# Performance work log

Hardware: AMD Instinct MI355X
Metric: run time of the kernel (lower is better)

## Reference

```python
import jax, jax.numpy as jnp
import numpy as np

N = 4096
HIDDEN = 256
NUM_HEADS = 8
HEAD_DIM = HIDDEN // NUM_HEADS
LN_EPS = 1e-3


def setup_inputs() -> dict:
    key = jax.random.key(0)
    ks = jax.random.split(key, 8)
    s = 1.0 / np.sqrt(HIDDEN)
    feat = jax.random.normal(ks[0], (N, HIDDEN), dtype=jnp.float32)
    Wq = jax.random.normal(ks[1], (HIDDEN, HIDDEN), dtype=jnp.float32) * s
    bq = jnp.zeros((HIDDEN,), dtype=jnp.float32)
    Wkv = jax.random.normal(ks[2], (HIDDEN, 2 * HIDDEN), dtype=jnp.float32) * s
    bkv = jnp.zeros((2 * HIDDEN,), dtype=jnp.float32)
    Weg = jax.random.normal(ks[3], (HIDDEN, 2 * NUM_HEADS), dtype=jnp.float32) * s
    beg = jnp.zeros((2 * NUM_HEADS,), dtype=jnp.float32)
    ln_g = jnp.ones((HIDDEN,), dtype=jnp.float32)
    ln_b = jnp.zeros((HIDDEN,), dtype=jnp.float32)
    return {"feat": feat, "Wq": Wq, "bq": bq, "Wkv": Wkv, "bkv": bkv,
            "Weg": Weg, "beg": beg, "ln_g": ln_g, "ln_b": ln_b}


def reference(feat, Wq, bq, Wkv, bkv, Weg, beg, ln_g, ln_b):
    n = feat.shape[0]
    # projections
    Q = feat @ Wq + bq                                  # [N, hidden]
    KV = feat @ Wkv + bkv                               # [N, 2*hidden]
    K, V = jnp.split(KV, 2, axis=-1)
    EG = feat @ Weg + beg                               # [N, 2*heads]
    E, G = jnp.split(EG, 2, axis=-1)                    # each [N, heads]
    # reshape to [N, head_dim, heads] (heads is the FAST axis, as in torch .view)
    Q = Q.reshape(n, HEAD_DIM, NUM_HEADS) * (HEAD_DIM ** -0.5)
    K = K.reshape(n, HEAD_DIM, NUM_HEADS)
    V = V.reshape(n, HEAD_DIM, NUM_HEADS)
    # all-pairs scores with per-j edge bias: [N, N, heads]
    H = jnp.einsum('idh,jdh->ijh', Q, K) + E[None, :, :]
    # softmax over i (axis 0), post-softmax sigmoid gate (per j, h)
    A = jax.nn.softmax(H, axis=0) * jax.nn.sigmoid(G)[None, :, :]
    Va = jnp.einsum('ijh,jdh->idh', A, V).reshape(n, HIDDEN)
    # layernorm eps=1e-3
    mu = jnp.mean(Va, axis=-1, keepdims=True)
    var = jnp.var(Va, axis=-1, keepdims=True)
    return (Va - mu) * jax.lax.rsqrt(var + LN_EPS) * ln_g + ln_b
```

## Files before the change

kernel.cpp:

```cpp
#include <hip/hip_runtime.h>
#include <hip/hip_bf16.h>

#define N 4096
#define HID 256
#define NH 8
#define HD 32
#define NC 784
#define CH 16
#define JSPAN (N / CH)

typedef __attribute__((ext_vector_type(8))) short short8;
typedef __attribute__((ext_vector_type(4))) short short4v;
typedef __attribute__((ext_vector_type(4))) float f32x4;
typedef __attribute__((ext_vector_type(2))) unsigned int uint2v;
typedef __attribute__((ext_vector_type(4))) unsigned int uint4v;

#define QSCALE 0.25503482f

static __device__ __forceinline__ unsigned short f2bf(float f) {
    union { float f; unsigned u; } v; v.f = f;
    unsigned r = v.u + 0x7fff + ((v.u >> 16) & 1);
    return (unsigned short)(r >> 16);
}
static __device__ __forceinline__ float bf2f(unsigned short u) {
    union { unsigned u; float f; } v; v.u = ((unsigned)u) << 16; return v.f;
}
static __device__ __forceinline__ unsigned packhu(float a, float b) {
    unsigned ua = __builtin_bit_cast(unsigned, a) + 0x8000u;
    unsigned ub = __builtin_bit_cast(unsigned, b) + 0x8000u;
    return __builtin_amdgcn_perm(ub, ua, 0x07060302u);
}

__global__ void k_prep(const float* __restrict__ feat, const float* __restrict__ Wq,
                       const float* __restrict__ Wkv, const float* __restrict__ Weg,
                       const float* __restrict__ bq, const float* __restrict__ bkv,
                       const float* __restrict__ beg, unsigned short* __restrict__ featb,
                       unsigned short* __restrict__ WbT, float* __restrict__ bC,
                       float* __restrict__ colS) {
    int bx = blockIdx.x;
    if (bx < 1024) {
        int t = bx * 256 + threadIdx.x;
        float4 v = ((const float4*)feat)[t];
        short4v o;
        o[0] = (short)f2bf(v.x); o[1] = (short)f2bf(v.y);
        o[2] = (short)f2bf(v.z); o[3] = (short)f2bf(v.w);
        ((short4v*)featb)[t] = o;
    } else {
        int c = bx - 1024, k = threadIdx.x;
        float w, b;
        if (c < 256)      { w = Wq[k * 256 + c];          b = bq[c]; }
        else if (c < 768) { w = Wkv[k * 512 + (c - 256)]; b = bkv[c - 256]; }
        else              { w = Weg[k * 16 + (c - 768)];  b = beg[c - 768]; }
        WbT[c * 256 + k] = f2bf(w);
        if (k == 0) bC[c] = b;
        if (c < 128) colS[c * 256 + k] = 0.f;
    }
}

__global__ __launch_bounds__(256) void k_proj(const unsigned short* __restrict__ featb,
                                              const unsigned short* __restrict__ WbT,
                                              const float* __restrict__ bC,
                                              unsigned short* __restrict__ Qp,
                                              unsigned short* __restrict__ Kp,
                                              unsigned short* __restrict__ VpT,
                                              float* __restrict__ sigG) {
    int w = threadIdx.x >> 6, l = threadIdx.x & 63;
    int il = l & 15, g = l >> 4;
    int c0 = blockIdx.x * 16;
    int i0 = (blockIdx.y * 4 + w) * 16;
    const short8* Arow = (const short8*)(featb + (size_t)(i0 + il) * HID);
    const short8* Brow = (const short8*)(WbT + (size_t)(c0 + il) * HID);
    f32x4 acc = {0.f, 0.f, 0.f, 0.f};
#pragma unroll
    for (int k0 = 0; k0 < HID; k0 += 32) {
        short8 a = Arow[(k0 >> 3) + g];
        short8 b = Brow[(k0 >> 3) + g];
        acc = __builtin_amdgcn_mfma_f32_16x16x32_bf16(a, b, acc, 0, 0, 0);
    }
    int c = c0 + il;
    float bias = bC[c];
#pragma unroll
    for (int r = 0; r < 4; ++r) {
        int i = i0 + g * 4 + r;
        float val = acc[r] + bias;
        if (c < 256) {
            int h = c & 7, d = c >> 3;
            Qp[((size_t)h * N + i) * HD + d] = f2bf(val * QSCALE);
        } else if (c < 512) {
            int cc = c - 256, h = cc & 7, d = cc >> 3;
            Kp[((size_t)h * N + i) * HD + d] = f2bf(val);
        } else if (c < 768) {
            int cc = c - 512, h = cc & 7, d = cc >> 3;
            VpT[((size_t)h * HD + d) * N + i] = f2bf(val);
        } else {
            int cc = c - 768;
            if (cc >= 8) sigG[(size_t)(cc - 8) * N + i] = 1.f / (1.f + __expf(-val));
        }
    }
}

__global__ __launch_bounds__(256) void k_pass1(const unsigned short* __restrict__ Qp,
                                               const unsigned short* __restrict__ Kp,
                                               float* __restrict__ colS) {
    int w = threadIdx.x >> 6, l = threadIdx.x & 63;
    int il = l & 15, g = l >> 4;
    int h = blockIdx.y;
    int j0 = (blockIdx.x * 4 + w) * 64;
    const unsigned short* Kh = Kp + (size_t)h * N * HD;
    short8 Kf[4];
#pragma unroll
    for (int t = 0; t < 4; ++t)
        Kf[t] = *(const short8*)(Kh + (size_t)(j0 + 16 * t + il) * HD + g * 8);
    const unsigned short* Qh = Qp + (size_t)h * N * HD;
    f32x4 z = {0.f, 0.f, 0.f, 0.f};
    float s[4] = {0.f, 0.f, 0.f, 0.f};
    int ibeg = blockIdx.z * 128;
    short8 Qa0 = *(const short8*)(Qh + (size_t)(ibeg + il) * HD + g * 8);
    short8 Qb0 = *(const short8*)(Qh + (size_t)(ibeg + 16 + il) * HD + g * 8);
    short8 Qa1 = *(const short8*)(Qh + (size_t)(ibeg + 32 + il) * HD + g * 8);
    short8 Qb1 = *(const short8*)(Qh + (size_t)(ibeg + 48 + il) * HD + g * 8);
#pragma unroll
    for (int it = 0; it < 4; ++it) {
        int i0 = ibeg + it * 32;
        short8 cQa = Qa0, cQb = Qb0;
        Qa0 = Qa1; Qb0 = Qb1;
        int in = i0 + 64;
        Qa1 = *(const short8*)(Qh + (size_t)(in + il) * HD + g * 8);
        Qb1 = *(const short8*)(Qh + (size_t)(in + 16 + il) * HD + g * 8);
        __builtin_amdgcn_sched_barrier(0);
#pragma unroll
        for (int t = 0; t < 4; ++t) {
            f32x4 Sa = __builtin_amdgcn_mfma_f32_16x16x32_bf16(cQa, Kf[t], z, 0, 0, 0);
            f32x4 Sb = __builtin_amdgcn_mfma_f32_16x16x32_bf16(cQb, Kf[t], z, 0, 0, 0);
            s[t] += ((__builtin_amdgcn_exp2f(Sa[0]) + __builtin_amdgcn_exp2f(Sa[1]))
                   + (__builtin_amdgcn_exp2f(Sa[2]) + __builtin_amdgcn_exp2f(Sa[3])))
                  + ((__builtin_amdgcn_exp2f(Sb[0]) + __builtin_amdgcn_exp2f(Sb[1]))
                   + (__builtin_amdgcn_exp2f(Sb[2]) + __builtin_amdgcn_exp2f(Sb[3])));
        }
    }
#pragma unroll
    for (int t = 0; t < 4; ++t) {
        s[t] += __shfl_xor(s[t], 16);
        s[t] += __shfl_xor(s[t], 32);
    }
    if (g == 0) {
#pragma unroll
        for (int t = 0; t < 4; ++t)
            atomicAdd(&colS[(size_t)h * N + j0 + 16 * t + il], s[t]);
    }
}

__global__ void k_vprep(unsigned short* __restrict__ VpT,
                        const float* __restrict__ sigG,
                        const float* __restrict__ colS) {
    int row = blockIdx.x >> 1;
    int j0 = ((blockIdx.x & 1) * 256 + threadIdx.x) * 8;
    int h = row >> 5;
    unsigned short* p = VpT + (size_t)row * N + j0;
    short8 v = *(short8*)p;
    const float* sg = sigG + (size_t)h * N + j0;
    const float* cs = colS + (size_t)h * N + j0;
    f32x4 sa = *(const f32x4*)sg, sb = *(const f32x4*)(sg + 4);
    f32x4 ca = *(const f32x4*)cs, cb = *(const f32x4*)(cs + 4);
    uint4v ov;
    ov[0] = packhu(bf2f((unsigned short)v[0]) * sa[0] / ca[0],
                   bf2f((unsigned short)v[1]) * sa[1] / ca[1]);
    ov[1] = packhu(bf2f((unsigned short)v[2]) * sa[2] / ca[2],
                   bf2f((unsigned short)v[3]) * sa[3] / ca[3]);
    ov[2] = packhu(bf2f((unsigned short)v[4]) * sb[0] / cb[0],
                   bf2f((unsigned short)v[5]) * sb[1] / cb[1]);
    ov[3] = packhu(bf2f((unsigned short)v[6]) * sb[2] / cb[2],
                   bf2f((unsigned short)v[7]) * sb[3] / cb[3]);
    *(uint4v*)p = ov;
}

static __device__ __forceinline__ short8 frag_dance(f32x4 Sa, f32x4 Sb) {
    unsigned A0 = packhu(__builtin_amdgcn_exp2f(Sa[0]), __builtin_amdgcn_exp2f(Sa[1]));
    unsigned A1 = packhu(__builtin_amdgcn_exp2f(Sa[2]), __builtin_amdgcn_exp2f(Sa[3]));
    unsigned B0 = packhu(__builtin_amdgcn_exp2f(Sb[0]), __builtin_amdgcn_exp2f(Sb[1]));
    unsigned B1 = packhu(__builtin_amdgcn_exp2f(Sb[2]), __builtin_amdgcn_exp2f(Sb[3]));
    uint2v r1 = __builtin_amdgcn_permlane32_swap(A0, B0, false, false);
    uint2v r2 = __builtin_amdgcn_permlane16_swap(r1[0], r1[1], false, false);
    uint2v r3 = __builtin_amdgcn_permlane32_swap(A1, B1, false, false);
    uint2v r4 = __builtin_amdgcn_permlane16_swap(r3[0], r3[1], false, false);
    uint4v pu;
    pu[0] = r2[0]; pu[1] = r4[0]; pu[2] = r2[1]; pu[3] = r4[1];
    return __builtin_bit_cast(short8, pu);
}

__global__ __launch_bounds__(128) void k_pass2(const unsigned short* __restrict__ Qp,
                                               const unsigned short* __restrict__ Kp,
                                               const unsigned short* __restrict__ VpT,
                                               unsigned short* __restrict__ Vpb) {
    int w = threadIdx.x >> 6, l = threadIdx.x & 63;
    int il = l & 15, g = l >> 4;
    int h = blockIdx.y;
    int i0 = blockIdx.x * 128 + w * 64;
    int jbeg = blockIdx.z * JSPAN;
    const unsigned short* Qh = Qp + (size_t)h * N * HD;
    const unsigned short* Kh = Kp + ((size_t)h * N + jbeg) * HD;
    const unsigned short* Vh = VpT + (size_t)h * HD * N + jbeg;
    short8 Qf[4];
#pragma unroll
    for (int q = 0; q < 4; ++q)
        Qf[q] = *(const short8*)(Qh + (size_t)(i0 + q * 16 + il) * HD + g * 8);
    f32x4 z = {0.f, 0.f, 0.f, 0.f};
    f32x4 acc[4][2];
#pragma unroll
    for (int q = 0; q < 4; ++q) { acc[q][0] = z; acc[q][1] = z; }
    short8 K0a = *(const short8*)(Kh + (size_t)il * HD + g * 8);
    short8 K1a = *(const short8*)(Kh + (size_t)(16 + il) * HD + g * 8);
    short8 V0a = *(const short8*)(Vh + (size_t)il * N + g * 8);
    short8 V1a = *(const short8*)(Vh + (size_t)(16 + il) * N + g * 8);
    short8 K0b = *(const short8*)(Kh + (size_t)(32 + il) * HD + g * 8);
    short8 K1b = *(const short8*)(Kh + (size_t)(48 + il) * HD + g * 8);
    short8 V0b = *(const short8*)(Vh + (size_t)il * N + 32 + g * 8);
    short8 V1b = *(const short8*)(Vh + (size_t)(16 + il) * N + 32 + g * 8);
#pragma unroll
    for (int it = 0; it < 8; ++it) {
        int jb = it * 32;
        short8 cK0 = K0a, cK1 = K1a, cV0 = V0a, cV1 = V1a;
        K0a = K0b; K1a = K1b; V0a = V0b; V1a = V1b;
        int jn = jb + 64;
        K0b = *(const short8*)(Kh + (size_t)(jn + il) * HD + g * 8);
        K1b = *(const short8*)(Kh + (size_t)(jn + 16 + il) * HD + g * 8);
        V0b = *(const short8*)(Vh + (size_t)il * N + jn + g * 8);
        V1b = *(const short8*)(Vh + (size_t)(16 + il) * N + jn + g * 8);
        __builtin_amdgcn_sched_barrier(0);
#pragma unroll
        for (int q = 0; q < 4; ++q) {
            f32x4 SA = __builtin_amdgcn_mfma_f32_16x16x32_bf16(cK0, Qf[q], z, 0, 0, 0);
            f32x4 SB = __builtin_amdgcn_mfma_f32_16x16x32_bf16(cK1, Qf[q], z, 0, 0, 0);
            short8 Pa = frag_dance(SA, SB);
            acc[q][0] = __builtin_amdgcn_mfma_f32_16x16x32_bf16(Pa, cV0, acc[q][0], 0, 0, 0);
            acc[q][1] = __builtin_amdgcn_mfma_f32_16x16x32_bf16(Pa, cV1, acc[q][1], 0, 0, 0);
        }
    }
    unsigned short* Vout = Vpb + (size_t)(blockIdx.z * NH + h) * N * HD;
#pragma unroll
    for (int q = 0; q < 4; ++q) {
#pragma unroll
        for (int r = 0; r < 4; ++r) {
            int ia = i0 + q * 16 + g * 4 + r;
            Vout[(size_t)ia * HD + il]      = f2bf(acc[q][0][r]);
            Vout[(size_t)ia * HD + 16 + il] = f2bf(acc[q][1][r]);
        }
    }
}

__global__ __launch_bounds__(256) void k_ln(const unsigned short* __restrict__ Vpb,
                                            const float* __restrict__ gam,
                                            const float* __restrict__ bet,
                                            float* __restrict__ out) {
    int w = threadIdx.x >> 6, l = threadIdx.x & 63;
    int i = blockIdx.x * 4 + w;
    int h = l >> 3, d0 = (l & 7) << 2;
    f32x4 x = {0.f, 0.f, 0.f, 0.f};
#pragma unroll
    for (int c = 0; c < CH; ++c) {
        short4v v = *(const short4v*)(Vpb + ((size_t)(c * NH + h) * N + i) * HD + d0);
        x[0] += bf2f((unsigned short)v[0]); x[1] += bf2f((unsigned short)v[1]);
        x[2] += bf2f((unsigned short)v[2]); x[3] += bf2f((unsigned short)v[3]);
    }
    float s1 = x[0] + x[1] + x[2] + x[3];
    float s2 = x[0] * x[0] + x[1] * x[1] + x[2] * x[2] + x[3] * x[3];
#pragma unroll
    for (int off = 1; off < 64; off <<= 1) {
        s1 += __shfl_xor(s1, off);
        s2 += __shfl_xor(s2, off);
    }
    float mu = s1 * (1.f / 256.f);
    float var = s2 * (1.f / 256.f) - mu * mu;
    float rs = rsqrtf(var + 1e-3f);
#pragma unroll
    for (int r = 0; r < 4; ++r) {
        int c = (d0 + r) * 8 + h;
        out[(size_t)i * HID + c] = (x[r] - mu) * rs * gam[c] + bet[c];
    }
}

extern "C" void kernel_launch(void* const* d_in, const int* in_sizes, int n_in,
                              void* d_out, int out_size, void* d_ws, size_t ws_size,
                              hipStream_t stream) {
    const float* feat = (const float*)d_in[0];
    const float* Wq   = (const float*)d_in[1];
    const float* bq   = (const float*)d_in[2];
    const float* Wkv  = (const float*)d_in[3];
    const float* bkv  = (const float*)d_in[4];
    const float* Weg  = (const float*)d_in[5];
    const float* beg  = (const float*)d_in[6];
    const float* ln_g = (const float*)d_in[7];
    const float* ln_b = (const float*)d_in[8];
    float* out = (float*)d_out;

    char* ws = (char*)d_ws;
    unsigned short* Qp    = (unsigned short*)(ws + 0);
    unsigned short* Kp    = (unsigned short*)(ws + (2u << 20));
    unsigned short* VpT   = (unsigned short*)(ws + (4u << 20));
    unsigned short* featb = (unsigned short*)(ws + (6u << 20));
    unsigned short* WbT   = (unsigned short*)(ws + (8u << 20));
    float* bC   = (float*)(ws + (8u << 20) + (512u << 10));
    float* sigG = (float*)(ws + (8u << 20) + (528u << 10));
    float* colS = (float*)(ws + (8u << 20) + (656u << 10));
    unsigned short* Vpb = (unsigned short*)(ws + (9u << 20));

    k_prep<<<dim3(1024 + NC), 256, 0, stream>>>(feat, Wq, Wkv, Weg, bq, bkv, beg,
                                                featb, WbT, bC, colS);
    k_proj<<<dim3(49, 64), 256, 0, stream>>>(featb, WbT, bC, Qp, Kp, VpT, sigG);
    k_pass1<<<dim3(16, NH, 32), 256, 0, stream>>>(Qp, Kp, colS);
    k_vprep<<<dim3(512), 256, 0, stream>>>(VpT, sigG, colS);
    k_pass2<<<dim3(32, NH, CH), 128, 0, stream>>>(Qp, Kp, VpT, Vpb);
    k_ln<<<dim3(1024), 256, 0, stream>>>(Vpb, ln_g, ln_b, out);
}
```

Baseline: 100.3 us.

## Fuse V scaling into pass2 and stage K/V tiles in swizzled LDS

Removes the separate k_vprep kernel and folds the V * sigmoid(G) / colsum scaling into k_pass2's prologue. Each block now has 256 threads covering 256 query rows, and it stages its whole K and scaled-V j-span in XOR-swizzled shared memory instead of streaming per-wave register prefetches from global memory. This saves one launch and a global read/write pass over V, and lets four waves share each K/V tile. The cost is a serial load phase plus a barrier before the MFMA loop, the loss of the software-pipelined global prefetch, and the scaling being recomputed by each of the 16 i-blocks.

Result: slower. 102.5 us (+2.2%).

```diff
diff --git a/kernel.cpp b/kernel.cpp
--- a/kernel.cpp
+++ b/kernel.cpp
@@ -150,30 +150,6 @@
     }
 }
 
-__global__ void k_vprep(unsigned short* __restrict__ VpT,
-                        const float* __restrict__ sigG,
-                        const float* __restrict__ colS) {
-    int row = blockIdx.x >> 1;
-    int j0 = ((blockIdx.x & 1) * 256 + threadIdx.x) * 8;
-    int h = row >> 5;
-    unsigned short* p = VpT + (size_t)row * N + j0;
-    short8 v = *(short8*)p;
-    const float* sg = sigG + (size_t)h * N + j0;
-    const float* cs = colS + (size_t)h * N + j0;
-    f32x4 sa = *(const f32x4*)sg, sb = *(const f32x4*)(sg + 4);
-    f32x4 ca = *(const f32x4*)cs, cb = *(const f32x4*)(cs + 4);
-    uint4v ov;
-    ov[0] = packhu(bf2f((unsigned short)v[0]) * sa[0] / ca[0],
-                   bf2f((unsigned short)v[1]) * sa[1] / ca[1]);
-    ov[1] = packhu(bf2f((unsigned short)v[2]) * sa[2] / ca[2],
-                   bf2f((unsigned short)v[3]) * sa[3] / ca[3]);
-    ov[2] = packhu(bf2f((unsigned short)v[4]) * sb[0] / cb[0],
-                   bf2f((unsigned short)v[5]) * sb[1] / cb[1]);
-    ov[3] = packhu(bf2f((unsigned short)v[6]) * sb[2] / cb[2],
-                   bf2f((unsigned short)v[7]) * sb[3] / cb[3]);
-    *(uint4v*)p = ov;
-}
-
 static __device__ __forceinline__ short8 frag_dance(f32x4 Sa, f32x4 Sb) {
     unsigned A0 = packhu(__builtin_amdgcn_exp2f(Sa[0]), __builtin_amdgcn_exp2f(Sa[1]));
     unsigned A1 = packhu(__builtin_amdgcn_exp2f(Sa[2]), __builtin_amdgcn_exp2f(Sa[3]));
@@ -188,45 +164,71 @@
     return __builtin_bit_cast(short8, pu);
 }
 
-__global__ __launch_bounds__(128) void k_pass2(const unsigned short* __restrict__ Qp,
+__global__ __launch_bounds__(256) void k_pass2(const unsigned short* __restrict__ Qp,
                                                const unsigned short* __restrict__ Kp,
                                                const unsigned short* __restrict__ VpT,
+                                               const float* __restrict__ sigG,
+                                               const float* __restrict__ colS,
                                                unsigned short* __restrict__ Vpb) {
+    __shared__ __align__(16) char KsB[256 * 64];
+    __shared__ __align__(16) char VsB[32 * 512];
     int w = threadIdx.x >> 6, l = threadIdx.x & 63;
     int il = l & 15, g = l >> 4;
     int h = blockIdx.y;
-    int i0 = blockIdx.x * 128 + w * 64;
+    int i0 = blockIdx.x * 256 + w * 64;
     int jbeg = blockIdx.z * JSPAN;
+    {
+        const unsigned short* Kg = Kp + ((size_t)h * N + jbeg) * HD;
+        int t = threadIdx.x;
+#pragma unroll
+        for (int p = 0; p < 4; ++p) {
+            int cidx = t + p * 256;
+            int j = cidx >> 2, ds = cidx & 3;
+            uint4v val = *(const uint4v*)(Kg + (size_t)j * HD + ds * 8);
+            *(uint4v*)(KsB + ((j * 64 + ds * 16) ^ ((j & 7) << 4))) = val;
+        }
+        const unsigned short* Vg = VpT + (size_t)h * HD * N + jbeg;
+        const float* sg = sigG + (size_t)h * N + jbeg;
+        const float* cs = colS + (size_t)h * N + jbeg;
+#pragma unroll
+        for (int p = 0; p < 4; ++p) {
+            int cidx = t + p * 256;
+            int d = cidx >> 5, j0 = (cidx & 31) * 8;
+            short8 v = *(const short8*)(Vg + (size_t)d * N + j0);
+            f32x4 s0 = *(const f32x4*)(sg + j0), s1 = *(const f32x4*)(sg + j0 + 4);
+            f32x4 c0 = *(const f32x4*)(cs + j0), c1 = *(const f32x4*)(cs + j0 + 4);
+            uint4v o;
+            o[0] = packhu(bf2f((unsigned short)v[0]) * s0[0] / c0[0],
+                          bf2f((unsigned short)v[1]) * s0[1] / c0[1]);
+            o[1] = packhu(bf2f((unsigned short)v[2]) * s0[2] / c0[2],
+                          bf2f((unsigned short)v[3]) * s0[3] / c0[3]);
+            o[2] = packhu(bf2f((unsigned short)v[4]) * s1[0] / c1[0],
+                          bf2f((unsigned short)v[5]) * s1[1] / c1[1]);
+            o[3] = packhu(bf2f((unsigned short)v[6]) * s1[2] / c1[2],
+                          bf2f((unsigned short)v[7]) * s1[3] / c1[3]);
+            *(uint4v*)(VsB + ((d * 512 + j0 * 2) ^ ((d & 7) << 4))) = o;
+        }
+    }
     const unsigned short* Qh = Qp + (size_t)h * N * HD;
-    const unsigned short* Kh = Kp + ((size_t)h * N + jbeg) * HD;
-    const unsigned short* Vh = VpT + (size_t)h * HD * N + jbeg;
     short8 Qf[4];
 #pragma unroll
     for (int q = 0; q < 4; ++q)
         Qf[q] = *(const short8*)(Qh + (size_t)(i0 + q * 16 + il) * HD + g * 8);
+    __syncthreads();
     f32x4 z = {0.f, 0.f, 0.f, 0.f};
     f32x4 acc[4][2];
 #pragma unroll
     for (int q = 0; q < 4; ++q) { acc[q][0] = z; acc[q][1] = z; }
-    short8 K0a = *(const short8*)(Kh + (size_t)il * HD + g * 8);
-    short8 K1a = *(const short8*)(Kh + (size_t)(16 + il) * HD + g * 8);
-    short8 V0a = *(const short8*)(Vh + (size_t)il * N + g * 8);
-    short8 V1a = *(const short8*)(Vh + (size_t)(16 + il) * N + g * 8);
-    short8 K0b = *(const short8*)(Kh + (size_t)(32 + il) * HD + g * 8);
-    short8 K1b = *(const short8*)(Kh + (size_t)(48 + il) * HD + g * 8);
-    short8 V0b = *(const short8*)(Vh + (size_t)il * N + 32 + g * 8);
-    short8 V1b = *(const short8*)(Vh + (size_t)(16 + il) * N + 32 + g * 8);
+    int sw = (il & 7) << 4;
+    int kA = (il * 64 + g * 16) ^ sw;
 #pragma unroll
     for (int it = 0; it < 8; ++it) {
         int jb = it * 32;
-        short8 cK0 = K0a, cK1 = K1a, cV0 = V0a, cV1 = V1a;
-        K0a = K0b; K1a = K1b; V0a = V0b; V1a = V1b;
-        int jn = jb + 64;
-        K0b = *(const short8*)(Kh + (size_t)(jn + il) * HD + g * 8);
-        K1b = *(const short8*)(Kh + (size_t)(jn + 16 + il) * HD + g * 8);
-        V0b = *(const short8*)(Vh + (size_t)il * N + jn + g * 8);
-        V1b = *(const short8*)(Vh + (size_t)(16 + il) * N + jn + g * 8);
-        __builtin_amdgcn_sched_barrier(0);
+        short8 cK0 = *(const short8*)(KsB + jb * 64 + kA);
+        short8 cK1 = *(const short8*)(KsB + jb * 64 + 1024 + kA);
+        int vo = (jb * 2 + g * 16) ^ sw;
+        short8 cV0 = *(const short8*)(VsB + il * 512 + vo);
+        short8 cV1 = *(const short8*)(VsB + il * 512 + 8192 + vo);
 #pragma unroll
         for (int q = 0; q < 4; ++q) {
             f32x4 SA = __builtin_amdgcn_mfma_f32_16x16x32_bf16(cK0, Qf[q], z, 0, 0, 0);
@@ -308,7 +310,6 @@
                                                 featb, WbT, bC, colS);
     k_proj<<<dim3(49, 64), 256, 0, stream>>>(featb, WbT, bC, Qp, Kp, VpT, sigG);
     k_pass1<<<dim3(16, NH, 32), 256, 0, stream>>>(Qp, Kp, colS);
-    k_vprep<<<dim3(512), 256, 0, stream>>>(VpT, sigG, colS);
-    k_pass2<<<dim3(32, NH, CH), 128, 0, stream>>>(Qp, Kp, VpT, Vpb);
+    k_pass2<<<dim3(16, NH, CH), 256, 0, stream>>>(Qp, Kp, VpT, sigG, colS, Vpb);
     k_ln<<<dim3(1024), 256, 0, stream>>>(Vpb, ln_g, ln_b, out);
 }
```
